# Optimization experiments

Measured on AMD Instinct MI355X. Metric: run time of the kernel, lower is better.

## Reference

```python
import jax, jax.numpy as jnp
from jax import lax
import numpy as np


def _lstm_layer(x, W_ih, W_hh, b_ih, b_hh):
    # x: (T, B, in_dim); gate order i, f, g, o (PyTorch convention)
    T, B, _ = x.shape
    H = W_hh.shape[1]
    # precompute input projections for all timesteps (one big GEMM)
    x_proj = jnp.einsum('tbi,gi->tbg', x, W_ih) + b_ih + b_hh  # (T, B, 4H)

    def step(carry, xt):
        h, c = carry
        gates = xt + h @ W_hh.T  # (B, 4H)
        i, f, g, o = jnp.split(gates, 4, axis=-1)
        c = jax.nn.sigmoid(f) * c + jax.nn.sigmoid(i) * jnp.tanh(g)
        h = jax.nn.sigmoid(o) * jnp.tanh(c)
        return (h, c), h

    h0 = jnp.zeros((B, H), dtype=x.dtype)
    c0 = jnp.zeros((B, H), dtype=x.dtype)
    (hT, cT), hs = lax.scan(step, (h0, c0), x_proj)
    return hs, hT, cT


def setup_inputs() -> dict:
    key = jax.random.key(0)
    ks = jax.random.split(key, 12)
    T, B, D_in, H, D_out = 1024, 64, 256, 512, 256
    s_in = 1.0 / np.sqrt(H)
    inp = {
        'x': jax.random.normal(ks[0], (T, B, D_in), jnp.float32),
        'W_ih0': jax.random.uniform(ks[1], (4 * H, D_in), jnp.float32, -s_in, s_in),
        'W_hh0': jax.random.uniform(ks[2], (4 * H, H), jnp.float32, -s_in, s_in),
        'b_ih0': jax.random.uniform(ks[3], (4 * H,), jnp.float32, -s_in, s_in),
        'b_hh0': jax.random.uniform(ks[4], (4 * H,), jnp.float32, -s_in, s_in),
        'W_ih1': jax.random.uniform(ks[5], (4 * H, H), jnp.float32, -s_in, s_in),
        'W_hh1': jax.random.uniform(ks[6], (4 * H, H), jnp.float32, -s_in, s_in),
        'b_ih1': jax.random.uniform(ks[7], (4 * H,), jnp.float32, -s_in, s_in),
        'b_hh1': jax.random.uniform(ks[8], (4 * H,), jnp.float32, -s_in, s_in),
        'W_out': jax.random.uniform(ks[9], (D_out, H), jnp.float32, -s_in, s_in),
        'b_out': jax.random.uniform(ks[10], (D_out,), jnp.float32, -s_in, s_in),
    }
    return inp


def reference(x, W_ih0, W_hh0, b_ih0, b_hh0, W_ih1, W_hh1, b_ih1, b_hh1, W_out, b_out):
    h1s, h1, c1 = _lstm_layer(x, W_ih0, W_hh0, b_ih0, b_hh0)
    h2s, h2, c2 = _lstm_layer(h1s, W_ih1, W_hh1, b_ih1, b_hh1)
    out = jnp.einsum('tbh,oh->tbo', h2s, W_out) + b_out  # (T, B, D_out)
    hn = jnp.stack([h1, h2], axis=0)  # (num_layers, B, H)
    cn = jnp.stack([c1, c2], axis=0)
    return (out, hn, cn)
```

## Files before the change

kernel.cpp:

```cpp
#include <hip/hip_runtime.h>

#define TT   1024
#define BB   64
#define DIN  256
#define HH   512
#define DOUT 256

#define NWG_L0  64
#define NWG_L1  128
#define NWG_OUT 8
#define NWG_TOT 200

typedef short bf16x8 __attribute__((ext_vector_type(8)));
typedef float f32x4  __attribute__((ext_vector_type(4)));
typedef unsigned u32x4 __attribute__((ext_vector_type(4)));

__device__ bf16x8 g_xf[TT * 2048];
__device__ bf16x8 g_h1f[4][4096];
__device__ bf16x8 g_h2f[4][4096];
__device__ bf16x8 g_h1z[4096];
__device__ bf16x8 g_h2z[4096];

__device__ unsigned g_flg[520 * 16];
__device__ unsigned g_iter;

__device__ __forceinline__ unsigned* FLG(int idx) { return &g_flg[idx * 16]; }

__device__ __forceinline__ u32x4 ldg_cv16(const void* p) {
    u32x4 r;
    asm volatile("global_load_dwordx4 %0, %1, off sc0 sc1"
                 : "=&v"(r) : "v"(p) : "memory");
    return r;
}
__device__ __forceinline__ void stg_cv16(void* p, u32x4 v) {
    asm volatile("global_store_dwordx4 %0, %1, off sc0 sc1" :: "v"(p), "v"(v) : "memory");
}
__device__ __forceinline__ void stg_cv_u32(void* p, unsigned v) {
    asm volatile("global_store_dword %0, %1, off sc0 sc1" :: "v"(p), "v"(v) : "memory");
}
__device__ __forceinline__ void wait_vm0(void) {
    asm volatile("s_waitcnt vmcnt(0)" ::: "memory");
}

__device__ __forceinline__ void waitpoll(const unsigned* p, unsigned tgt, int active, int tid) {
    for (;;) {
        unsigned v = 0xFFFFFFFFu;
        if (active)
            asm volatile("global_load_dword %0, %1, off sc0 sc1\n\t"
                         "s_waitcnt vmcnt(0)"
                         : "=&v"(v) : "v"(p) : "memory");
        if (__all(v >= tgt)) break;
        __builtin_amdgcn_s_sleep(1);
    }
    __syncthreads();
}

__device__ __forceinline__ float sigf(float v) { return 1.f / (1.f + __expf(-v)); }
__device__ __forceinline__ float tanh_fast(float v) { return 2.f / (1.f + __expf(-2.f * v)) - 1.f; }

__device__ __forceinline__ short f2bf(float f) {
    unsigned u = __builtin_bit_cast(unsigned, f);
    unsigned r = (u + 0x7FFFu + ((u >> 16) & 1u)) >> 16;
    return (short)r;
}

__device__ __forceinline__ bf16x8 pack8(float4 v0, float4 v1) {
    bf16x8 r;
    r[0] = f2bf(v0.x); r[1] = f2bf(v0.y); r[2] = f2bf(v0.z); r[3] = f2bf(v0.w);
    r[4] = f2bf(v1.x); r[5] = f2bf(v1.y); r[6] = f2bf(v1.z); r[7] = f2bf(v1.w);
    return r;
}

extern "C" __global__ void __launch_bounds__(256)
pack_x(const float* __restrict__ x) {
    const int t = blockIdx.x, tid = threadIdx.x;
    const float* xt = x + (size_t)t * BB * DIN;
    bf16x8* dst = g_xf + (size_t)t * 2048;
    #pragma unroll
    for (int u = 0; u < 8; ++u) {
        const int f = u * 256 + tid;
        const int lane_ = f & 63, ctks = f >> 6;
        const int ct = ctks & 3, ks = ctks >> 2;
        const int b  = ct * 16 + (lane_ & 15);
        const int kb = ks * 32 + (lane_ >> 4) * 8;
        const float4* s = (const float4*)(xt + b * DIN + kb);
        dst[f] = pack8(s[0], s[1]);
    }
}

template<int L, int NCT>
__device__ void run_layer(int lwg, int tid,
                          const float* __restrict__ wih, const float* __restrict__ whh,
                          const float* __restrict__ bih, const float* __restrict__ bhh,
                          float* __restrict__ out, unsigned Q, bf16x8* sB, short* sH)
{
    constexpr int KINX = (L == 0) ? DIN : HH;
    constexpr int NKSA = KINX / 32;
    constexpr int NKS  = NKSA + HH / 32;
    constexpr int NSTA = NKSA * NCT / 4;
    constexpr int NSTB = (HH / 32) * NCT / 4;

    const int lane = tid & 63, lo = lane & 15, hi = lane >> 4;
    const int w      = tid >> 6;
    const int ctbase = (NCT == 2) ? (lwg & 1) * 2 : (lwg & 3);
    const int grp    = (NCT == 2) ? (lwg & 1) : (lwg & 3);
    const int ub     = (NCT == 2) ? (lwg >> 1) : (lwg >> 2);
    const int wv     = ub * 4 + w;
    const int jbase  = wv * 4;
    const int grow   = (lo & 3) * HH + jbase + (lo >> 2);

    bf16x8 aF[NKS];
    #pragma unroll
    for (int ks = 0; ks < NKS; ++ks) {
        const float* wr;
        if (ks < NKSA) wr = wih + (size_t)grow * KINX + ks * 32 + hi * 8;
        else           wr = whh + (size_t)grow * HH + (ks - NKSA) * 32 + hi * 8;
        const float4* p = (const float4*)wr;
        aF[ks] = pack8(p[0], p[1]);
    }

    f32x4 biasv;
    #pragma unroll
    for (int r = 0; r < 4; ++r)
        biasv[r] = bih[r * HH + jbase + hi] + bhh[r * HH + jbase + hi];

    const unsigned Qb = Q * 2048u;
    float cst[NCT];
    #pragma unroll
    for (int c = 0; c < NCT; ++c) cst[c] = 0.f;

    for (int t = 0; t < TT; ++t) {
        const bf16x8* srcA = (L == 0) ? (g_xf + (size_t)t * 2048) : g_h1f[t & 3];
        const bf16x8* srcB = (L == 0) ? ((t == 0) ? g_h1z : g_h1f[(t - 1) & 3])
                                      : ((t == 0) ? g_h2z : g_h2f[(t - 1) & 3]);

        if (L == 1) {
            const unsigned* wp = g_flg; unsigned wt = 0; int wa = 0;
            if (w == 0 && lane < 32) { wp = FLG(0 + (grp >> 1) * 32 + lane);
                                       wt = Qb + t + 1; wa = 1; }
            waitpoll(wp, wt, wa, tid);
        }

        u32x4 stgA[NSTA];
        #pragma unroll
        for (int r = 0; r < NSTA; ++r) {
            const int ri = r * 4 + w, ks = ri / NCT, c = ri % NCT;
            const bf16x8* src = &srcA[(ks * 4 + ctbase + c) * 64 + lane];
            if (L == 0) stgA[r] = *(const u32x4*)src;
            else        stgA[r] = ldg_cv16(src);
        }
        wait_vm0();
        #pragma unroll
        for (int r = 0; r < NSTA; ++r)
            ((u32x4*)sB)[(r * 4 + w) * 64 + lane] = stgA[r];

        {
            const unsigned* wp = g_flg; unsigned wt = 0; int wa = 0;
            if (w == 0 && lane < 32 && t >= 1) {
                wp = (L == 0) ? FLG(0 + grp * 32 + lane) : FLG(64 + grp * 32 + lane);
                wt = Qb + t; wa = 1;
            }
            waitpoll(wp, wt, wa, tid);
        }
        if (L == 1 && tid == 0) stg_cv_u32(FLG(192 + grp * 32 + ub), Qb + t + 1);

        u32x4 stgB[NSTB];
        #pragma unroll
        for (int r = 0; r < NSTB; ++r) {
            const int ri = r * 4 + w, ks = ri / NCT, c = ri % NCT;
            stgB[r] = ldg_cv16(&srcB[(ks * 4 + ctbase + c) * 64 + lane]);
        }
        f32x4 acc[NCT];
        #pragma unroll
        for (int c = 0; c < NCT; ++c) acc[c] = biasv;
        #pragma unroll
        for (int ks = 0; ks < NKSA; ++ks)
            #pragma unroll
            for (int c = 0; c < NCT; ++c)
                acc[c] = __builtin_amdgcn_mfma_f32_16x16x32_bf16(
                    aF[ks], sB[(ks * NCT + c) * 64 + lane], acc[c], 0, 0, 0);
        wait_vm0();
        #pragma unroll
        for (int r = 0; r < NSTB; ++r)
            ((u32x4*)sB)[(NKSA * NCT + r * 4 + w) * 64 + lane] = stgB[r];
        __syncthreads();
        if (tid == 0) {
            if (L == 0) stg_cv_u32(FLG(320 + grp * 32 + ub), Qb + t);
            else        stg_cv_u32(FLG(384 + grp * 32 + ub), Qb + t);
        }
        #pragma unroll
        for (int ks = NKSA; ks < NKS; ++ks)
            #pragma unroll
            for (int c = 0; c < NCT; ++c)
                acc[c] = __builtin_amdgcn_mfma_f32_16x16x32_bf16(
                    aF[ks], sB[(ks * NCT + c) * 64 + lane], acc[c], 0, 0, 0);

        #pragma unroll
        for (int c = 0; c < NCT; ++c) {
            const float gi = acc[c][0], gf = acc[c][1];
            const float gg = acc[c][2], go = acc[c][3];
            const float cn_ = sigf(gf) * cst[c] + sigf(gi) * tanh_fast(gg);
            const float hv  = sigf(go) * tanh_fast(cn_);
            cst[c] = cn_;
            sH[((c * 2 + (w >> 1)) * 16 + lo) * 8 + (w & 1) * 4 + hi] = f2bf(hv);
            if (t == TT - 1) {
                const int j = jbase + hi, b = (ctbase + c) * 16 + lo;
                const size_t base = (size_t)TT * BB * DOUT;
                out[base + (size_t)L * BB * HH + (size_t)b * HH + j] = hv;
                out[base + (size_t)2 * BB * HH + (size_t)L * BB * HH + (size_t)b * HH + j] = cn_;
            }
        }

        {
            const unsigned* wp = g_flg; unsigned wt = 0; int wa = 0;
            if (t >= 4) {
                if (L == 0) {
                    if (w == 1) { wp = FLG(192 + (grp * 2 + (lane >> 5)) * 32 + (lane & 31));
                                  wt = Qb + t - 3; wa = 1; }
                    else if (w == 2 && lane < 32) { wp = FLG(320 + grp * 32 + lane);
                                                    wt = Qb + t - 3; wa = 1; }
                } else {
                    if (w == 1) {
                        if (lane < 32)      { wp = FLG(384 + grp * 32 + lane);
                                              wt = Qb + t - 3; wa = 1; }
                        else if (lane < 36) { wp = FLG(512 + (grp >> 1) * 4 + (lane - 32));
                                              wt = Qb + t - 3; wa = 1; }
                    }
                }
            }
            waitpoll(wp, wt, wa, tid);
        }

        u32x4* ringW = (u32x4*)((L == 0) ? g_h1f[t & 3] : g_h2f[t & 3]);
        if (tid < 32 * NCT) {
            const int c = tid >> 5, r = tid & 31, hi2 = r >> 4, lo2 = r & 15;
            const int f = ((ub >> 1) * 4 + ctbase + c) * 64 + ((ub & 1) * 2 + hi2) * 16 + lo2;
            stg_cv16(ringW + f, *(const u32x4*)&sH[((c * 2 + hi2) * 16 + lo2) * 8]);
        }
        wait_vm0();
        if (tid == 0) {
            if (L == 0) stg_cv_u32(FLG(0 + grp * 32 + ub), Qb + t + 1);
            else        stg_cv_u32(FLG(64 + grp * 32 + ub), Qb + t + 1);
        }
    }
}

__device__ void run_out(int lwg, int tid,
                        const float* __restrict__ wout, const float* __restrict__ bout,
                        float* __restrict__ out, unsigned Q, bf16x8* sB)
{
    constexpr int NKS  = HH / 32;
    constexpr int NST  = 8;
    const int lane = tid & 63, lo = lane & 15, hi = lane >> 4;
    const int w = tid >> 6;
    const int cp = lwg & 1, ob = lwg >> 1;
    const int ctbase = cp * 2;
    const int obase = (ob * 4 + w) * 16;
    const unsigned Qb = Q * 2048u;

    bf16x8 aF[NKS];
    #pragma unroll
    for (int ks = 0; ks < NKS; ++ks) {
        const float4* p = (const float4*)(wout + (size_t)(obase + lo) * HH + ks * 32 + hi * 8);
        aF[ks] = pack8(p[0], p[1]);
    }
    f32x4 biasv;
    #pragma unroll
    for (int r = 0; r < 4; ++r) biasv[r] = bout[obase + hi * 4 + r];

    for (int t = 0; t < TT; ++t) {
        const unsigned* wp = g_flg; unsigned wt = 0; int wa = 0;
        if (w == 0) {
            wp = FLG(64 + (ctbase + (lane >> 5)) * 32 + (lane & 31));
            wt = Qb + t + 1; wa = 1;
        }
        waitpoll(wp, wt, wa, tid);

        const bf16x8* src = g_h2f[t & 3];
        u32x4 stg[NST];
        #pragma unroll
        for (int r = 0; r < NST; ++r) {
            const int ri = r * 4 + w;
            const int ks = ri >> 1, c = ri & 1;
            stg[r] = ldg_cv16(&src[(ks * 4 + ctbase + c) * 64 + lane]);
        }
        wait_vm0();
        #pragma unroll
        for (int r = 0; r < NST; ++r)
            ((u32x4*)sB)[(r * 4 + w) * 64 + lane] = stg[r];
        __syncthreads();
        if (tid == 0) stg_cv_u32(FLG(512 + cp * 4 + ob), Qb + t + 1);

        f32x4 acc[2] = {biasv, biasv};
        #pragma unroll
        for (int ks = 0; ks < NKS; ++ks)
            #pragma unroll
            for (int c = 0; c < 2; ++c)
                acc[c] = __builtin_amdgcn_mfma_f32_16x16x32_bf16(
                    aF[ks], sB[(ks * 2 + c) * 64 + lane], acc[c], 0, 0, 0);
        #pragma unroll
        for (int c = 0; c < 2; ++c)
            #pragma unroll
            for (int r = 0; r < 4; ++r) {
                const int b = (ctbase + c) * 16 + lo, o = obase + hi * 4 + r;
                out[(size_t)t * BB * DOUT + (size_t)b * DOUT + o] = acc[c][r];
            }
    }
}

extern "C" __global__ void __launch_bounds__(256, 1)
lstm2_fused(const float* __restrict__ x,
            const float* __restrict__ wih0, const float* __restrict__ whh0,
            const float* __restrict__ bih0, const float* __restrict__ bhh0,
            const float* __restrict__ wih1, const float* __restrict__ whh1,
            const float* __restrict__ bih1, const float* __restrict__ bhh1,
            const float* __restrict__ wout, const float* __restrict__ bout,
            float* __restrict__ out)
{
    __shared__ bf16x8 sB[3072];
    __shared__ __align__(16) short sH[2 * 2 * 16 * 8];

    const int tid = threadIdx.x, wg = blockIdx.x;
    const unsigned Q = __hip_atomic_load(&g_iter, __ATOMIC_RELAXED, __HIP_MEMORY_SCOPE_AGENT);

    if (wg < NWG_L0)
        run_layer<0, 2>(wg, tid, wih0, whh0, bih0, bhh0, out, Q, sB, sH);
    else if (wg < NWG_L0 + NWG_L1)
        run_layer<1, 1>(wg - NWG_L0, tid, wih1, whh1, bih1, bhh1, out, Q, sB, sH);
    else
        run_out(wg - NWG_L0 - NWG_L1, tid, wout, bout, out, Q, sB);

    if (wg == 0 && tid == 0)
        __hip_atomic_store(&g_iter, Q + 1, __ATOMIC_RELAXED, __HIP_MEMORY_SCOPE_AGENT);
}

extern "C" void kernel_launch(void* const* d_in, const int* in_sizes, int n_in,
                              void* d_out, int out_size, void* d_ws, size_t ws_size,
                              hipStream_t stream) {
    const float* x    = (const float*)d_in[0];
    const float* wih0 = (const float*)d_in[1];
    const float* whh0 = (const float*)d_in[2];
    const float* bih0 = (const float*)d_in[3];
    const float* bhh0 = (const float*)d_in[4];
    const float* wih1 = (const float*)d_in[5];
    const float* whh1 = (const float*)d_in[6];
    const float* bih1 = (const float*)d_in[7];
    const float* bhh1 = (const float*)d_in[8];
    const float* wout = (const float*)d_in[9];
    const float* bout = (const float*)d_in[10];
    float* out = (float*)d_out;

    hipLaunchKernelGGL(pack_x, dim3(TT), dim3(256), 0, stream, x);
    hipLaunchKernelGGL(lstm2_fused, dim3(NWG_TOT), dim3(256), 0, stream,
                       x, wih0, whh0, bih0, bhh0, wih1, whh1, bih1, bhh1,
                       wout, bout, out);
}
```

Before: 3.705 ms.

## Halve workgroup count by giving each wave two hidden-unit tiles

Each wave now owns 8 hidden units (two 4-unit MFMA tiles) instead of 4, so the persistent kernel runs 100 workgroups instead of 200 and keeps twice the weights in registers. The flag layout and wait points are reorganised: the ring-buffer and flag waits move to the top of each step, and the h stores are written as whole contiguous tiles after extra barriers. The output projection workgroups each cover all 64 batch rows. This reduces the number of per-step cross-workgroup flag polls and syncs, at the cost of more MFMA work and register pressure per wave, plus added __syncthreads.

```diff
diff --git a/kernel.cpp b/kernel.cpp
--- a/kernel.cpp
+++ b/kernel.cpp
@@ -6,10 +6,10 @@
 #define HH   512
 #define DOUT 256
 
-#define NWG_L0  64
-#define NWG_L1  128
-#define NWG_OUT 8
-#define NWG_TOT 200
+#define NWG_L0  32
+#define NWG_L1  64
+#define NWG_OUT 4
+#define NWG_TOT 100
 
 typedef short bf16x8 __attribute__((ext_vector_type(8)));
 typedef float f32x4  __attribute__((ext_vector_type(4)));
@@ -21,7 +21,7 @@
 __device__ bf16x8 g_h1z[4096];
 __device__ bf16x8 g_h2z[4096];
 
-__device__ unsigned g_flg[520 * 16];
+__device__ unsigned g_flg[260 * 16];
 __device__ unsigned g_iter;
 
 __device__ __forceinline__ unsigned* FLG(int idx) { return &g_flg[idx * 16]; }
@@ -88,58 +88,84 @@
     }
 }
 
-template<int L, int NCT>
+template<int L>
 __device__ void run_layer(int lwg, int tid,
                           const float* __restrict__ wih, const float* __restrict__ whh,
                           const float* __restrict__ bih, const float* __restrict__ bhh,
                           float* __restrict__ out, unsigned Q, bf16x8* sB, short* sH)
 {
+    constexpr int NCT  = (L == 0) ? 2 : 1;
     constexpr int KINX = (L == 0) ? DIN : HH;
     constexpr int NKSA = KINX / 32;
-    constexpr int NKS  = NKSA + HH / 32;
+    constexpr int NKSB = HH / 32;
+    constexpr int NKS  = NKSA + NKSB;
     constexpr int NSTA = NKSA * NCT / 4;
-    constexpr int NSTB = (HH / 32) * NCT / 4;
+    constexpr int NSTB = NKSB * NCT / 4;
 
     const int lane = tid & 63, lo = lane & 15, hi = lane >> 4;
     const int w      = tid >> 6;
-    const int ctbase = (NCT == 2) ? (lwg & 1) * 2 : (lwg & 3);
-    const int grp    = (NCT == 2) ? (lwg & 1) : (lwg & 3);
-    const int ub     = (NCT == 2) ? (lwg >> 1) : (lwg >> 2);
-    const int wv     = ub * 4 + w;
-    const int jbase  = wv * 4;
-    const int grow   = (lo & 3) * HH + jbase + (lo >> 2);
-
-    bf16x8 aF[NKS];
-    #pragma unroll
-    for (int ks = 0; ks < NKS; ++ks) {
-        const float* wr;
-        if (ks < NKSA) wr = wih + (size_t)grow * KINX + ks * 32 + hi * 8;
-        else           wr = whh + (size_t)grow * HH + (ks - NKSA) * 32 + hi * 8;
-        const float4* p = (const float4*)wr;
-        aF[ks] = pack8(p[0], p[1]);
-    }
-
-    f32x4 biasv;
-    #pragma unroll
-    for (int r = 0; r < 4; ++r)
-        biasv[r] = bih[r * HH + jbase + hi] + bhh[r * HH + jbase + hi];
+    const int grp    = (L == 0) ? (lwg & 1) : (lwg & 3);
+    const int ub     = (L == 0) ? (lwg >> 1) : (lwg >> 2);
+    const int ctbase = (L == 0) ? grp * 2 : grp;
+    const int jbase  = ub * 32 + w * 8;
+
+    bf16x8 aF[NKS][2];
+    #pragma unroll
+    for (int ks = 0; ks < NKS; ++ks)
+        #pragma unroll
+        for (int q = 0; q < 2; ++q) {
+            const int grow = (lo & 3) * HH + jbase + q * 4 + (lo >> 2);
+            const float* wr = (ks < NKSA)
+                ? wih + (size_t)grow * KINX + ks * 32 + hi * 8
+                : whh + (size_t)grow * HH + (ks - NKSA) * 32 + hi * 8;
+            const float4* p = (const float4*)wr;
+            aF[ks][q] = pack8(p[0], p[1]);
+        }
+
+    f32x4 biasv[2];
+    #pragma unroll
+    for (int q = 0; q < 2; ++q)
+        #pragma unroll
+        for (int r = 0; r < 4; ++r)
+            biasv[q][r] = bih[r * HH + jbase + q * 4 + hi] + bhh[r * HH + jbase + q * 4 + hi];
 
     const unsigned Qb = Q * 2048u;
-    float cst[NCT];
-    #pragma unroll
-    for (int c = 0; c < NCT; ++c) cst[c] = 0.f;
+    float cst[2][NCT];
+    #pragma unroll
+    for (int q = 0; q < 2; ++q)
+        #pragma unroll
+        for (int c = 0; c < NCT; ++c) cst[q][c] = 0.f;
 
     for (int t = 0; t < TT; ++t) {
+        {
+            const unsigned* wp = g_flg; unsigned wt = 0; int wa = 0;
+            if (L == 0) {
+                if (w == 0) { if (lane < 16 && t >= 1) { wp = FLG(0 + grp * 16 + lane);
+                                                         wt = Qb + t; wa = 1; } }
+                else if (w == 1 && t >= 4) {
+                    if (lane < 16)      { wp = FLG(96 + (2 * grp) * 16 + lane);
+                                          wt = Qb + t - 3; wa = 1; }
+                    else if (lane < 32) { wp = FLG(96 + (2 * grp + 1) * 16 + (lane - 16));
+                                          wt = Qb + t - 3; wa = 1; }
+                    else if (lane < 48) { wp = FLG(160 + grp * 16 + (lane - 32));
+                                          wt = Qb + t - 3; wa = 1; }
+                }
+            } else {
+                if (w == 0) { if (lane < 16) { wp = FLG(0 + (grp >> 1) * 16 + lane);
+                                               wt = Qb + t + 1; wa = 1; } }
+                else if (w == 1 && t >= 4) {
+                    if (lane < 16)      { wp = FLG(192 + grp * 16 + lane);
+                                          wt = Qb + t - 3; wa = 1; }
+                    else if (lane < 20) { wp = FLG(256 + (lane - 16));
+                                          wt = Qb + t - 3; wa = 1; }
+                }
+            }
+            waitpoll(wp, wt, wa, tid);
+        }
+
         const bf16x8* srcA = (L == 0) ? (g_xf + (size_t)t * 2048) : g_h1f[t & 3];
         const bf16x8* srcB = (L == 0) ? ((t == 0) ? g_h1z : g_h1f[(t - 1) & 3])
                                       : ((t == 0) ? g_h2z : g_h2f[(t - 1) & 3]);
-
-        if (L == 1) {
-            const unsigned* wp = g_flg; unsigned wt = 0; int wa = 0;
-            if (w == 0 && lane < 32) { wp = FLG(0 + (grp >> 1) * 32 + lane);
-                                       wt = Qb + t + 1; wa = 1; }
-            waitpoll(wp, wt, wa, tid);
-        }
 
         u32x4 stgA[NSTA];
         #pragma unroll
@@ -153,16 +179,15 @@
         #pragma unroll
         for (int r = 0; r < NSTA; ++r)
             ((u32x4*)sB)[(r * 4 + w) * 64 + lane] = stgA[r];
-
-        {
+        __syncthreads();
+        if (L == 1 && tid == 0) stg_cv_u32(FLG(96 + grp * 16 + ub), Qb + t + 1);
+
+        if (L == 1) {
             const unsigned* wp = g_flg; unsigned wt = 0; int wa = 0;
-            if (w == 0 && lane < 32 && t >= 1) {
-                wp = (L == 0) ? FLG(0 + grp * 32 + lane) : FLG(64 + grp * 32 + lane);
-                wt = Qb + t; wa = 1;
-            }
+            if (w == 0 && lane < 16 && t >= 1) { wp = FLG(32 + grp * 16 + lane);
+                                                 wt = Qb + t; wa = 1; }
             waitpoll(wp, wt, wa, tid);
         }
-        if (L == 1 && tid == 0) stg_cv_u32(FLG(192 + grp * 32 + ub), Qb + t + 1);
 
         u32x4 stgB[NSTB];
         #pragma unroll
@@ -170,139 +195,125 @@
             const int ri = r * 4 + w, ks = ri / NCT, c = ri % NCT;
             stgB[r] = ldg_cv16(&srcB[(ks * 4 + ctbase + c) * 64 + lane]);
         }
-        f32x4 acc[NCT];
-        #pragma unroll
-        for (int c = 0; c < NCT; ++c) acc[c] = biasv;
+        f32x4 acc[2][NCT];
+        #pragma unroll
+        for (int q = 0; q < 2; ++q)
+            #pragma unroll
+            for (int c = 0; c < NCT; ++c) acc[q][c] = biasv[q];
         #pragma unroll
         for (int ks = 0; ks < NKSA; ++ks)
             #pragma unroll
-            for (int c = 0; c < NCT; ++c)
-                acc[c] = __builtin_amdgcn_mfma_f32_16x16x32_bf16(
-                    aF[ks], sB[(ks * NCT + c) * 64 + lane], acc[c], 0, 0, 0);
+            for (int q = 0; q < 2; ++q)
+                #pragma unroll
+                for (int c = 0; c < NCT; ++c)
+                    acc[q][c] = __builtin_amdgcn_mfma_f32_16x16x32_bf16(
+                        aF[ks][q], sB[(ks * NCT + c) * 64 + lane], acc[q][c], 0, 0, 0);
         wait_vm0();
         #pragma unroll
         for (int r = 0; r < NSTB; ++r)
             ((u32x4*)sB)[(NKSA * NCT + r * 4 + w) * 64 + lane] = stgB[r];
         __syncthreads();
         if (tid == 0) {
-            if (L == 0) stg_cv_u32(FLG(320 + grp * 32 + ub), Qb + t);
-            else        stg_cv_u32(FLG(384 + grp * 32 + ub), Qb + t);
+            if (L == 0) stg_cv_u32(FLG(160 + grp * 16 + ub), Qb + t);
+            else        stg_cv_u32(FLG(192 + grp * 16 + ub), Qb + t);
         }
         #pragma unroll
         for (int ks = NKSA; ks < NKS; ++ks)
             #pragma unroll
-            for (int c = 0; c < NCT; ++c)
-                acc[c] = __builtin_amdgcn_mfma_f32_16x16x32_bf16(
-                    aF[ks], sB[(ks * NCT + c) * 64 + lane], acc[c], 0, 0, 0);
-
-        #pragma unroll
-        for (int c = 0; c < NCT; ++c) {
-            const float gi = acc[c][0], gf = acc[c][1];
-            const float gg = acc[c][2], go = acc[c][3];
-            const float cn_ = sigf(gf) * cst[c] + sigf(gi) * tanh_fast(gg);
-            const float hv  = sigf(go) * tanh_fast(cn_);
-            cst[c] = cn_;
-            sH[((c * 2 + (w >> 1)) * 16 + lo) * 8 + (w & 1) * 4 + hi] = f2bf(hv);
-            if (t == TT - 1) {
-                const int j = jbase + hi, b = (ctbase + c) * 16 + lo;
-                const size_t base = (size_t)TT * BB * DOUT;
-                out[base + (size_t)L * BB * HH + (size_t)b * HH + j] = hv;
-                out[base + (size_t)2 * BB * HH + (size_t)L * BB * HH + (size_t)b * HH + j] = cn_;
-            }
-        }
-
-        {
-            const unsigned* wp = g_flg; unsigned wt = 0; int wa = 0;
-            if (t >= 4) {
-                if (L == 0) {
-                    if (w == 1) { wp = FLG(192 + (grp * 2 + (lane >> 5)) * 32 + (lane & 31));
-                                  wt = Qb + t - 3; wa = 1; }
-                    else if (w == 2 && lane < 32) { wp = FLG(320 + grp * 32 + lane);
-                                                    wt = Qb + t - 3; wa = 1; }
-                } else {
-                    if (w == 1) {
-                        if (lane < 32)      { wp = FLG(384 + grp * 32 + lane);
-                                              wt = Qb + t - 3; wa = 1; }
-                        else if (lane < 36) { wp = FLG(512 + (grp >> 1) * 4 + (lane - 32));
-                                              wt = Qb + t - 3; wa = 1; }
-                    }
+            for (int q = 0; q < 2; ++q)
+                #pragma unroll
+                for (int c = 0; c < NCT; ++c)
+                    acc[q][c] = __builtin_amdgcn_mfma_f32_16x16x32_bf16(
+                        aF[ks][q], sB[(ks * NCT + c) * 64 + lane], acc[q][c], 0, 0, 0);
+
+        #pragma unroll
+        for (int q = 0; q < 2; ++q)
+            #pragma unroll
+            for (int c = 0; c < NCT; ++c) {
+                const float gi = acc[q][c][0], gf = acc[q][c][1];
+                const float gg = acc[q][c][2], go = acc[q][c][3];
+                const float cn_ = sigf(gf) * cst[q][c] + sigf(gi) * tanh_fast(gg);
+                const float hv  = sigf(go) * tanh_fast(cn_);
+                cst[q][c] = cn_;
+                sH[((c * 64) + w * 16 + lo) * 8 + q * 4 + hi] = f2bf(hv);
+                if (t == TT - 1) {
+                    const int j = jbase + q * 4 + hi, b = (ctbase + c) * 16 + lo;
+                    const size_t base = (size_t)TT * BB * DOUT;
+                    out[base + (size_t)L * BB * HH + (size_t)b * HH + j] = hv;
+                    out[base + (size_t)2 * BB * HH + (size_t)L * BB * HH + (size_t)b * HH + j] = cn_;
                 }
             }
-            waitpoll(wp, wt, wa, tid);
-        }
+        __syncthreads();
 
         u32x4* ringW = (u32x4*)((L == 0) ? g_h1f[t & 3] : g_h2f[t & 3]);
-        if (tid < 32 * NCT) {
-            const int c = tid >> 5, r = tid & 31, hi2 = r >> 4, lo2 = r & 15;
-            const int f = ((ub >> 1) * 4 + ctbase + c) * 64 + ((ub & 1) * 2 + hi2) * 16 + lo2;
-            stg_cv16(ringW + f, *(const u32x4*)&sH[((c * 2 + hi2) * 16 + lo2) * 8]);
+        if (tid < 64 * NCT) {
+            const int c = tid >> 6, l = tid & 63;
+            stg_cv16(ringW + (ub * 4 + ctbase + c) * 64 + l,
+                     *(const u32x4*)&sH[(c * 64 + l) * 8]);
         }
         wait_vm0();
+        __syncthreads();
         if (tid == 0) {
-            if (L == 0) stg_cv_u32(FLG(0 + grp * 32 + ub), Qb + t + 1);
-            else        stg_cv_u32(FLG(64 + grp * 32 + ub), Qb + t + 1);
-        }
-    }
-}
-
-__device__ void run_out(int lwg, int tid,
+            if (L == 0) stg_cv_u32(FLG(0 + grp * 16 + ub), Qb + t + 1);
+            else        stg_cv_u32(FLG(32 + grp * 16 + ub), Qb + t + 1);
+        }
+    }
+}
+
+__device__ void run_out(int ob, int tid,
                         const float* __restrict__ wout, const float* __restrict__ bout,
                         float* __restrict__ out, unsigned Q, bf16x8* sB)
 {
-    constexpr int NKS  = HH / 32;
-    constexpr int NST  = 8;
+    constexpr int NKS = HH / 32;
+    constexpr int NST = 16;
     const int lane = tid & 63, lo = lane & 15, hi = lane >> 4;
     const int w = tid >> 6;
-    const int cp = lwg & 1, ob = lwg >> 1;
-    const int ctbase = cp * 2;
-    const int obase = (ob * 4 + w) * 16;
+    const int ow = ob * 64 + w * 16;
     const unsigned Qb = Q * 2048u;
 
     bf16x8 aF[NKS];
     #pragma unroll
     for (int ks = 0; ks < NKS; ++ks) {
-        const float4* p = (const float4*)(wout + (size_t)(obase + lo) * HH + ks * 32 + hi * 8);
+        const float4* p = (const float4*)(wout + (size_t)(ow + lo) * HH + ks * 32 + hi * 8);
         aF[ks] = pack8(p[0], p[1]);
     }
     f32x4 biasv;
     #pragma unroll
-    for (int r = 0; r < 4; ++r) biasv[r] = bout[obase + hi * 4 + r];
+    for (int r = 0; r < 4; ++r) biasv[r] = bout[ow + hi * 4 + r];
 
     for (int t = 0; t < TT; ++t) {
-        const unsigned* wp = g_flg; unsigned wt = 0; int wa = 0;
-        if (w == 0) {
-            wp = FLG(64 + (ctbase + (lane >> 5)) * 32 + (lane & 31));
-            wt = Qb + t + 1; wa = 1;
-        }
-        waitpoll(wp, wt, wa, tid);
-
+        {
+            const unsigned* wp = g_flg; unsigned wt = 0; int wa = 0;
+            if (w == 0) { wp = FLG(32 + (lane >> 4) * 16 + (lane & 15));
+                          wt = Qb + t + 1; wa = 1; }
+            waitpoll(wp, wt, wa, tid);
+        }
         const bf16x8* src = g_h2f[t & 3];
         u32x4 stg[NST];
         #pragma unroll
         for (int r = 0; r < NST; ++r) {
             const int ri = r * 4 + w;
-            const int ks = ri >> 1, c = ri & 1;
-            stg[r] = ldg_cv16(&src[(ks * 4 + ctbase + c) * 64 + lane]);
+            stg[r] = ldg_cv16(&src[ri * 64 + lane]);
         }
         wait_vm0();
         #pragma unroll
         for (int r = 0; r < NST; ++r)
             ((u32x4*)sB)[(r * 4 + w) * 64 + lane] = stg[r];
         __syncthreads();
-        if (tid == 0) stg_cv_u32(FLG(512 + cp * 4 + ob), Qb + t + 1);
-
-        f32x4 acc[2] = {biasv, biasv};
+        if (tid == 0) stg_cv_u32(FLG(256 + ob), Qb + t + 1);
+
+        f32x4 acc[4] = {biasv, biasv, biasv, biasv};
         #pragma unroll
         for (int ks = 0; ks < NKS; ++ks)
             #pragma unroll
-            for (int c = 0; c < 2; ++c)
+            for (int c = 0; c < 4; ++c)
                 acc[c] = __builtin_amdgcn_mfma_f32_16x16x32_bf16(
-                    aF[ks], sB[(ks * 2 + c) * 64 + lane], acc[c], 0, 0, 0);
-        #pragma unroll
-        for (int c = 0; c < 2; ++c)
+                    aF[ks], sB[(ks * 4 + c) * 64 + lane], acc[c], 0, 0, 0);
+        #pragma unroll
+        for (int c = 0; c < 4; ++c)
             #pragma unroll
             for (int r = 0; r < 4; ++r) {
-                const int b = (ctbase + c) * 16 + lo, o = obase + hi * 4 + r;
+                const int b = c * 16 + lo, o = ow + hi * 4 + r;
                 out[(size_t)t * BB * DOUT + (size_t)b * DOUT + o] = acc[c][r];
             }
     }
@@ -317,16 +328,16 @@
             const float* __restrict__ wout, const float* __restrict__ bout,
             float* __restrict__ out)
 {
-    __shared__ bf16x8 sB[3072];
-    __shared__ __align__(16) short sH[2 * 2 * 16 * 8];
+    __shared__ bf16x8 sB[4096];
+    __shared__ __align__(16) short sH[2 * 64 * 8];
 
     const int tid = threadIdx.x, wg = blockIdx.x;
     const unsigned Q = __hip_atomic_load(&g_iter, __ATOMIC_RELAXED, __HIP_MEMORY_SCOPE_AGENT);
 
     if (wg < NWG_L0)
-        run_layer<0, 2>(wg, tid, wih0, whh0, bih0, bhh0, out, Q, sB, sH);
+        run_layer<0>(wg, tid, wih0, whh0, bih0, bhh0, out, Q, sB, sH);
     else if (wg < NWG_L0 + NWG_L1)
-        run_layer<1, 1>(wg - NWG_L0, tid, wih1, whh1, bih1, bhh1, out, Q, sB, sH);
+        run_layer<1>(wg - NWG_L0, tid, wih1, whh1, bih1, bhh1, out, Q, sB, sH);
     else
         run_out(wg - NWG_L0 - NWG_L1, tid, wout, bout, out, Q, sB);
 
```

Result: slower. 4.143 ms (+11.8%).

## Deepen hidden-state rings to 8 slots and batch backpressure polling per layer

Applied to the files above, without the earlier changes.

Grows the h1/h2 ring buffers from 4 to 8 slots and splits the templated layer routine into separate layer-0 and layer-1 versions. Layer 0 now loads x and its recurrent input together after a single poll. It checks consumer backpressure only every fourth step, folded into the same poll as the recurrent wait. Layer 1 moves its wait on layer 0 to the end of the previous step so that wait overlaps with other work. The aim is to cut per-step cross-workgroup flag polling latency on the serial recurrence, at the cost of more ring memory and an extra __syncthreads per step.

```diff
diff --git a/kernel.cpp b/kernel.cpp
--- a/kernel.cpp
+++ b/kernel.cpp
@@ -16,8 +16,8 @@
 typedef unsigned u32x4 __attribute__((ext_vector_type(4)));
 
 __device__ bf16x8 g_xf[TT * 2048];
-__device__ bf16x8 g_h1f[4][4096];
-__device__ bf16x8 g_h2f[4][4096];
+__device__ bf16x8 g_h1f[8][4096];
+__device__ bf16x8 g_h2f[8][4096];
 __device__ bf16x8 g_h1z[4096];
 __device__ bf16x8 g_h2z[4096];
 
@@ -88,108 +88,72 @@
     }
 }
 
-template<int L, int NCT>
-__device__ void run_layer(int lwg, int tid,
-                          const float* __restrict__ wih, const float* __restrict__ whh,
-                          const float* __restrict__ bih, const float* __restrict__ bhh,
-                          float* __restrict__ out, unsigned Q, bf16x8* sB, short* sH)
+__device__ void run_l0(int lwg, int tid,
+                       const float* __restrict__ wih, const float* __restrict__ whh,
+                       const float* __restrict__ bih, const float* __restrict__ bhh,
+                       float* __restrict__ out, unsigned Q, bf16x8* sB, short* sH)
 {
-    constexpr int KINX = (L == 0) ? DIN : HH;
-    constexpr int NKSA = KINX / 32;
-    constexpr int NKS  = NKSA + HH / 32;
-    constexpr int NSTA = NKSA * NCT / 4;
-    constexpr int NSTB = (HH / 32) * NCT / 4;
+    constexpr int NCT = 2, NKSA = DIN / 32, NKS = NKSA + HH / 32;
+    constexpr int NST = NKS * NCT / 4;
+    constexpr int NCXR = NKSA * NCT / 4;
 
     const int lane = tid & 63, lo = lane & 15, hi = lane >> 4;
-    const int w      = tid >> 6;
-    const int ctbase = (NCT == 2) ? (lwg & 1) * 2 : (lwg & 3);
-    const int grp    = (NCT == 2) ? (lwg & 1) : (lwg & 3);
-    const int ub     = (NCT == 2) ? (lwg >> 1) : (lwg >> 2);
-    const int wv     = ub * 4 + w;
-    const int jbase  = wv * 4;
-    const int grow   = (lo & 3) * HH + jbase + (lo >> 2);
+    const int w = tid >> 6;
+    const int grp = lwg & 1, ub = lwg >> 1;
+    const int ctbase = grp * 2;
+    const int wv = ub * 4 + w, jbase = wv * 4;
+    const int grow = (lo & 3) * HH + jbase + (lo >> 2);
 
     bf16x8 aF[NKS];
     #pragma unroll
     for (int ks = 0; ks < NKS; ++ks) {
-        const float* wr;
-        if (ks < NKSA) wr = wih + (size_t)grow * KINX + ks * 32 + hi * 8;
-        else           wr = whh + (size_t)grow * HH + (ks - NKSA) * 32 + hi * 8;
+        const float* wr = (ks < NKSA) ? wih + (size_t)grow * DIN + ks * 32 + hi * 8
+                                      : whh + (size_t)grow * HH + (ks - NKSA) * 32 + hi * 8;
         const float4* p = (const float4*)wr;
         aF[ks] = pack8(p[0], p[1]);
     }
-
     f32x4 biasv;
     #pragma unroll
     for (int r = 0; r < 4; ++r)
         biasv[r] = bih[r * HH + jbase + hi] + bhh[r * HH + jbase + hi];
 
     const unsigned Qb = Q * 2048u;
-    float cst[NCT];
-    #pragma unroll
-    for (int c = 0; c < NCT; ++c) cst[c] = 0.f;
+    float cst[NCT] = {0.f, 0.f};
 
     for (int t = 0; t < TT; ++t) {
-        const bf16x8* srcA = (L == 0) ? (g_xf + (size_t)t * 2048) : g_h1f[t & 3];
-        const bf16x8* srcB = (L == 0) ? ((t == 0) ? g_h1z : g_h1f[(t - 1) & 3])
-                                      : ((t == 0) ? g_h2z : g_h2f[(t - 1) & 3]);
-
-        if (L == 1) {
-            const unsigned* wp = g_flg; unsigned wt = 0; int wa = 0;
-            if (w == 0 && lane < 32) { wp = FLG(0 + (grp >> 1) * 32 + lane);
-                                       wt = Qb + t + 1; wa = 1; }
-            waitpoll(wp, wt, wa, tid);
-        }
-
-        u32x4 stgA[NSTA];
-        #pragma unroll
-        for (int r = 0; r < NSTA; ++r) {
-            const int ri = r * 4 + w, ks = ri / NCT, c = ri % NCT;
-            const bf16x8* src = &srcA[(ks * 4 + ctbase + c) * 64 + lane];
-            if (L == 0) stgA[r] = *(const u32x4*)src;
-            else        stgA[r] = ldg_cv16(src);
-        }
-        wait_vm0();
-        #pragma unroll
-        for (int r = 0; r < NSTA; ++r)
-            ((u32x4*)sB)[(r * 4 + w) * 64 + lane] = stgA[r];
-
         {
             const unsigned* wp = g_flg; unsigned wt = 0; int wa = 0;
-            if (w == 0 && lane < 32 && t >= 1) {
-                wp = (L == 0) ? FLG(0 + grp * 32 + lane) : FLG(64 + grp * 32 + lane);
-                wt = Qb + t; wa = 1;
-            }
+            const int bp = (t >= 8) && ((t & 3) == 0);
+            if (w == 0) { if (lane < 32 && t >= 1) { wp = FLG(0 + grp * 32 + lane);
+                                                     wt = Qb + t; wa = 1; } }
+            else if (w == 1) { if (bp) {
+                wp = FLG(192 + (grp * 2 + (lane >> 5)) * 32 + (lane & 31));
+                wt = Qb + t - 4; wa = 1; } }
+            else if (w == 2) { if (bp && lane < 32) {
+                wp = FLG(320 + grp * 32 + lane); wt = Qb + t - 4; wa = 1; } }
             waitpoll(wp, wt, wa, tid);
         }
-        if (L == 1 && tid == 0) stg_cv_u32(FLG(192 + grp * 32 + ub), Qb + t + 1);
-
-        u32x4 stgB[NSTB];
-        #pragma unroll
-        for (int r = 0; r < NSTB; ++r) {
+
+        const bf16x8* srcA = g_xf + (size_t)t * 2048;
+        const bf16x8* srcB = (t == 0) ? g_h1z : g_h1f[(t - 1) & 7];
+
+        u32x4 stg[NST];
+        #pragma unroll
+        for (int r = 0; r < NST; ++r) {
             const int ri = r * 4 + w, ks = ri / NCT, c = ri % NCT;
-            stgB[r] = ldg_cv16(&srcB[(ks * 4 + ctbase + c) * 64 + lane]);
-        }
-        f32x4 acc[NCT];
-        #pragma unroll
-        for (int c = 0; c < NCT; ++c) acc[c] = biasv;
-        #pragma unroll
-        for (int ks = 0; ks < NKSA; ++ks)
-            #pragma unroll
-            for (int c = 0; c < NCT; ++c)
-                acc[c] = __builtin_amdgcn_mfma_f32_16x16x32_bf16(
-                    aF[ks], sB[(ks * NCT + c) * 64 + lane], acc[c], 0, 0, 0);
-        wait_vm0();
-        #pragma unroll
-        for (int r = 0; r < NSTB; ++r)
-            ((u32x4*)sB)[(NKSA * NCT + r * 4 + w) * 64 + lane] = stgB[r];
-        __syncthreads();
-        if (tid == 0) {
-            if (L == 0) stg_cv_u32(FLG(320 + grp * 32 + ub), Qb + t);
-            else        stg_cv_u32(FLG(384 + grp * 32 + ub), Qb + t);
-        }
-        #pragma unroll
-        for (int ks = NKSA; ks < NKS; ++ks)
+            if (r < NCXR) stg[r] = *(const u32x4*)&srcA[(ks * 4 + ctbase + c) * 64 + lane];
+            else          stg[r] = ldg_cv16(&srcB[((ks - NKSA) * 4 + ctbase + c) * 64 + lane]);
+        }
+        wait_vm0();
+        #pragma unroll
+        for (int r = 0; r < NST; ++r)
+            ((u32x4*)sB)[(r * 4 + w) * 64 + lane] = stg[r];
+        __syncthreads();
+        if (tid == 0) stg_cv_u32(FLG(320 + grp * 32 + ub), Qb + t);
+
+        f32x4 acc[NCT] = {biasv, biasv};
+        #pragma unroll
+        for (int ks = 0; ks < NKS; ++ks)
             #pragma unroll
             for (int c = 0; c < NCT; ++c)
                 acc[c] = __builtin_amdgcn_mfma_f32_16x16x32_bf16(
@@ -206,41 +170,141 @@
             if (t == TT - 1) {
                 const int j = jbase + hi, b = (ctbase + c) * 16 + lo;
                 const size_t base = (size_t)TT * BB * DOUT;
-                out[base + (size_t)L * BB * HH + (size_t)b * HH + j] = hv;
-                out[base + (size_t)2 * BB * HH + (size_t)L * BB * HH + (size_t)b * HH + j] = cn_;
+                out[base + (size_t)b * HH + j] = hv;
+                out[base + (size_t)2 * BB * HH + (size_t)b * HH + j] = cn_;
             }
         }
-
-        {
-            const unsigned* wp = g_flg; unsigned wt = 0; int wa = 0;
-            if (t >= 4) {
-                if (L == 0) {
-                    if (w == 1) { wp = FLG(192 + (grp * 2 + (lane >> 5)) * 32 + (lane & 31));
-                                  wt = Qb + t - 3; wa = 1; }
-                    else if (w == 2 && lane < 32) { wp = FLG(320 + grp * 32 + lane);
-                                                    wt = Qb + t - 3; wa = 1; }
-                } else {
-                    if (w == 1) {
-                        if (lane < 32)      { wp = FLG(384 + grp * 32 + lane);
-                                              wt = Qb + t - 3; wa = 1; }
-                        else if (lane < 36) { wp = FLG(512 + (grp >> 1) * 4 + (lane - 32));
-                                              wt = Qb + t - 3; wa = 1; }
-                    }
-                }
-            }
-            waitpoll(wp, wt, wa, tid);
-        }
-
-        u32x4* ringW = (u32x4*)((L == 0) ? g_h1f[t & 3] : g_h2f[t & 3]);
-        if (tid < 32 * NCT) {
+        __syncthreads();
+
+        u32x4* ringW = (u32x4*)g_h1f[t & 7];
+        if (tid < 64) {
             const int c = tid >> 5, r = tid & 31, hi2 = r >> 4, lo2 = r & 15;
             const int f = ((ub >> 1) * 4 + ctbase + c) * 64 + ((ub & 1) * 2 + hi2) * 16 + lo2;
             stg_cv16(ringW + f, *(const u32x4*)&sH[((c * 2 + hi2) * 16 + lo2) * 8]);
         }
         wait_vm0();
-        if (tid == 0) {
-            if (L == 0) stg_cv_u32(FLG(0 + grp * 32 + ub), Qb + t + 1);
-            else        stg_cv_u32(FLG(64 + grp * 32 + ub), Qb + t + 1);
+        if (tid == 0) stg_cv_u32(FLG(0 + grp * 32 + ub), Qb + t + 1);
+    }
+}
+
+__device__ void run_l1(int lwg, int tid,
+                       const float* __restrict__ wih, const float* __restrict__ whh,
+                       const float* __restrict__ bih, const float* __restrict__ bhh,
+                       float* __restrict__ out, unsigned Q, bf16x8* sB, short* sH)
+{
+    constexpr int NKSA = HH / 32, NKS = 2 * NKSA;
+    constexpr int NSTA = NKSA / 4, NSTB = NKSA / 4;
+
+    const int lane = tid & 63, lo = lane & 15, hi = lane >> 4;
+    const int w = tid >> 6;
+    const int grp = lwg & 3, ub = lwg >> 2;
+    const int ctbase = grp;
+    const int wv = ub * 4 + w, jbase = wv * 4;
+    const int grow = (lo & 3) * HH + jbase + (lo >> 2);
+
+    bf16x8 aF[NKS];
+    #pragma unroll
+    for (int ks = 0; ks < NKS; ++ks) {
+        const float* wr = (ks < NKSA) ? wih + (size_t)grow * HH + ks * 32 + hi * 8
+                                      : whh + (size_t)grow * HH + (ks - NKSA) * 32 + hi * 8;
+        const float4* p = (const float4*)wr;
+        aF[ks] = pack8(p[0], p[1]);
+    }
+    f32x4 biasv;
+    #pragma unroll
+    for (int r = 0; r < 4; ++r)
+        biasv[r] = bih[r * HH + jbase + hi] + bhh[r * HH + jbase + hi];
+
+    const unsigned Qb = Q * 2048u;
+    float cst = 0.f;
+
+    {
+        const unsigned* wp = g_flg; unsigned wt = 0; int wa = 0;
+        if (w == 0 && lane < 32) { wp = FLG(0 + (grp >> 1) * 32 + lane); wt = Qb + 1; wa = 1; }
+        waitpoll(wp, wt, wa, tid);
+    }
+
+    for (int t = 0; t < TT; ++t) {
+        const bf16x8* srcA = g_h1f[t & 7];
+        const bf16x8* srcB = (t == 0) ? g_h2z : g_h2f[(t - 1) & 7];
+
+        u32x4 stgA[NSTA];
+        #pragma unroll
+        for (int r = 0; r < NSTA; ++r) {
+            const int ks = r * 4 + w;
+            stgA[r] = ldg_cv16(&srcA[(ks * 4 + ctbase) * 64 + lane]);
+        }
+        wait_vm0();
+        #pragma unroll
+        for (int r = 0; r < NSTA; ++r)
+            ((u32x4*)sB)[(r * 4 + w) * 64 + lane] = stgA[r];
+        __syncthreads();
+        if (tid == 0) stg_cv_u32(FLG(192 + grp * 32 + ub), Qb + t + 1);
+
+        {
+            const unsigned* wp = g_flg; unsigned wt = 0; int wa = 0;
+            if (w == 0 && lane < 32 && t >= 1) { wp = FLG(64 + grp * 32 + lane);
+                                                 wt = Qb + t; wa = 1; }
+            waitpoll(wp, wt, wa, tid);
+        }
+
+        u32x4 stgB[NSTB];
+        #pragma unroll
+        for (int r = 0; r < NSTB; ++r) {
+            const int ks = r * 4 + w;
+            stgB[r] = ldg_cv16(&srcB[(ks * 4 + ctbase) * 64 + lane]);
+        }
+        f32x4 acc = biasv;
+        #pragma unroll
+        for (int ks = 0; ks < NKSA; ++ks)
+            acc = __builtin_amdgcn_mfma_f32_16x16x32_bf16(
+                aF[ks], sB[ks * 64 + lane], acc, 0, 0, 0);
+        wait_vm0();
+        #pragma unroll
+        for (int r = 0; r < NSTB; ++r)
+            ((u32x4*)sB)[(NKSA + r * 4 + w) * 64 + lane] = stgB[r];
+        __syncthreads();
+        if (tid == 0) stg_cv_u32(FLG(384 + grp * 32 + ub), Qb + t);
+        #pragma unroll
+        for (int ks = NKSA; ks < NKS; ++ks)
+            acc = __builtin_amdgcn_mfma_f32_16x16x32_bf16(
+                aF[ks], sB[ks * 64 + lane], acc, 0, 0, 0);
+
+        {
+            const float gi = acc[0], gf = acc[1], gg = acc[2], go = acc[3];
+            const float cn_ = sigf(gf) * cst + sigf(gi) * tanh_fast(gg);
+            const float hv  = sigf(go) * tanh_fast(cn_);
+            cst = cn_;
+            sH[((w >> 1) * 16 + lo) * 8 + (w & 1) * 4 + hi] = f2bf(hv);
+            if (t == TT - 1) {
+                const int j = jbase + hi, b = ctbase * 16 + lo;
+                const size_t base = (size_t)TT * BB * DOUT;
+                out[base + (size_t)BB * HH + (size_t)b * HH + j] = hv;
+                out[base + (size_t)3 * BB * HH + (size_t)b * HH + j] = cn_;
+            }
+        }
+        __syncthreads();
+
+        u32x4* ringW = (u32x4*)g_h2f[t & 7];
+        if (tid < 32) {
+            const int hi2 = tid >> 4, lo2 = tid & 15;
+            const int f = ((ub >> 1) * 4 + ctbase) * 64 + ((ub & 1) * 2 + hi2) * 16 + lo2;
+            stg_cv16(ringW + f, *(const u32x4*)&sH[(hi2 * 16 + lo2) * 8]);
+        }
+        wait_vm0();
+        if (tid == 0) stg_cv_u32(FLG(64 + grp * 32 + ub), Qb + t + 1);
+
+        if (t < TT - 1) {
+            const unsigned* wp = g_flg; unsigned wt = 0; int wa = 0;
+            const int bp = (t >= 7) && ((t & 3) == 3);
+            if (w == 0) { if (lane < 32) { wp = FLG(0 + (grp >> 1) * 32 + lane);
+                                           wt = Qb + t + 2; wa = 1; } }
+            else if (w == 1) { if (bp) {
+                if (lane < 32)      { wp = FLG(384 + grp * 32 + lane);
+                                      wt = Qb + t - 3; wa = 1; }
+                else if (lane < 36) { wp = FLG(512 + (grp >> 1) * 4 + (lane - 32));
+                                      wt = Qb + t - 3; wa = 1; } } }
+            waitpoll(wp, wt, wa, tid);
         }
     }
 }
@@ -249,8 +313,8 @@
                         const float* __restrict__ wout, const float* __restrict__ bout,
                         float* __restrict__ out, unsigned Q, bf16x8* sB)
 {
-    constexpr int NKS  = HH / 32;
-    constexpr int NST  = 8;
+    constexpr int NKS = HH / 32;
+    constexpr int NST = 8;
     const int lane = tid & 63, lo = lane & 15, hi = lane >> 4;
     const int w = tid >> 6;
     const int cp = lwg & 1, ob = lwg >> 1;
@@ -276,7 +340,7 @@
         }
         waitpoll(wp, wt, wa, tid);
 
-        const bf16x8* src = g_h2f[t & 3];
+        const bf16x8* src = g_h2f[t & 7];
         u32x4 stg[NST];
         #pragma unroll
         for (int r = 0; r < NST; ++r) {
@@ -324,9 +388,9 @@
     const unsigned Q = __hip_atomic_load(&g_iter, __ATOMIC_RELAXED, __HIP_MEMORY_SCOPE_AGENT);
 
     if (wg < NWG_L0)
-        run_layer<0, 2>(wg, tid, wih0, whh0, bih0, bhh0, out, Q, sB, sH);
+        run_l0(wg, tid, wih0, whh0, bih0, bhh0, out, Q, sB, sH);
     else if (wg < NWG_L0 + NWG_L1)
-        run_layer<1, 1>(wg - NWG_L0, tid, wih1, whh1, bih1, bhh1, out, Q, sB, sH);
+        run_l1(wg - NWG_L0, tid, wih1, whh1, bih1, bhh1, out, Q, sB, sH);
     else
         run_out(wg - NWG_L0 - NWG_L1, tid, wout, bout, out, Q, sB);
 
```

After: 3.730 ms. About the same (+0.7%).
